# Kernel optimization log

Measured on AMD Instinct MI355X. Metric: run time of the kernel, lower is better.

Reference implementation:

```python
import jax, jax.numpy as jnp
import numpy as np

CNT_R = 500
DIM = 128
B, NEI = 8192, 64


def setup_inputs() -> dict:
    key = jax.random.key(0)
    ks = jax.random.split(key, 10)
    d2 = 2 * DIM
    return {
        "batch_nei_e_emb": jax.random.normal(ks[0], (B, NEI, DIM), dtype=jnp.float32),
        "batch_nei_rw": jax.random.uniform(ks[1], (B, NEI), dtype=jnp.float32),
        "w_r_table": jax.random.normal(ks[2], (2 * CNT_R + 1, DIM), dtype=jnp.float32),
        "zq_table": jax.random.normal(ks[3], (2 * CNT_R, DIM), dtype=jnp.float32),
        "attn_W_w": jax.random.normal(ks[4], (d2, d2), dtype=jnp.float32) / np.sqrt(d2),
        "attn_W_b": jnp.zeros((d2,), dtype=jnp.float32),
        "u_a_w": jax.random.normal(ks[5], (d2,), dtype=jnp.float32) / np.sqrt(d2),
        "u_a_b": jnp.zeros((), dtype=jnp.float32),
        "batch_nei_rid": jax.random.randint(ks[6], (B, NEI), 0, 2 * CNT_R + 1),
        "batch_q_rid": jax.random.randint(ks[7], (B,), 0, 2 * CNT_R),
    }


def reference(batch_nei_e_emb, batch_nei_rw, w_r_table, zq_table,
              attn_W_w, attn_W_b, u_a_w, u_a_b,
              batch_nei_rid, batch_q_rid):
    # gather relation hyperplane normals: (B, NEI, DIM)
    w_r = w_r_table[batch_nei_rid]
    n = w_r / jnp.linalg.norm(w_r, axis=-1, keepdims=True)
    # hyperplane projection: e - (e . n) n
    e = batch_nei_e_emb
    e_proj = e - jnp.sum(e * n, axis=-1, keepdims=True) * n
    # query relation embedding, tiled over neighbors: (B, NEI, DIM)
    z_q = zq_table[batch_q_rid]  # (B, DIM)
    z_q = jnp.broadcast_to(z_q[:, None, :], e_proj.shape)
    concat = jnp.concatenate([z_q, e_proj], axis=-1)  # (B, NEI, 2*DIM)
    h = jnp.tanh(jnp.einsum('bni,oi->bno', concat, attn_W_w) + attn_W_b)
    _alpha = jnp.einsum('bni,i->bn', h, u_a_w) + u_a_b  # (B, NEI)
    alpha = jax.nn.softmax(_alpha, axis=-1)
    attn = alpha + batch_nei_rw
    return attn
```

## Files before the change

kernel.cpp:

```cpp
#include <hip/hip_runtime.h>

#define NB    8192
#define NEI   64
#define DIM   128
#define D2    256
#define NR_W  1001
#define NR_Z  1000
#define EPB_LD 136

typedef __attribute__((ext_vector_type(8))) short bf16x8;
typedef __attribute__((ext_vector_type(4))) float f32x4;

__device__ __forceinline__ ushort f2bf(float x) {
    union { float f; unsigned u; } c; c.f = x;
    unsigned u = c.u;
    return (ushort)((u + 0x7fffu + ((u >> 16) & 1u)) >> 16);
}


__global__ void k_norm(const float* __restrict__ w_r_table, float* __restrict__ norm_t) {
    int r = blockIdx.x;
    int t = threadIdx.x;
    float v = w_r_table[r * DIM + t];
    float s = v * v;
    #pragma unroll
    for (int m = 1; m < 64; m <<= 1) s += __shfl_xor(s, m);
    __shared__ float sh[2];
    if ((t & 63) == 0) sh[t >> 6] = s;
    __syncthreads();
    float tot = sh[0] + sh[1];
    norm_t[r * DIM + t] = v / sqrtf(tot);
}

__global__ void k_tq(const float* __restrict__ zq_table, const float* __restrict__ W,
                     const float* __restrict__ bias, float* __restrict__ tq_t) {
    int r = blockIdx.x;
    int o = threadIdx.x;
    __shared__ float4 z4[32];
    if (o < 32) z4[o] = ((const float4*)(zq_table + r * DIM))[o];
    __syncthreads();
    const float4* wr = (const float4*)(W + o * D2);
    float acc = bias[o];
    #pragma unroll 8
    for (int i = 0; i < 32; ++i) {
        float4 wv = wr[i], zv = z4[i];
        acc += wv.x*zv.x + wv.y*zv.y + wv.z*zv.z + wv.w*zv.w;
    }
    tq_t[r * D2 + o] = acc;
}

__global__ void k_bfrag(const float* __restrict__ W, ushort* __restrict__ bfrag) {
    int nt = blockIdx.x;
    int kt = blockIdx.y;
    int l  = threadIdx.x;
    int o  = nt * 16 + (l & 15);
    int k  = kt * 32 + (l >> 4) * 8;
    const float4* src = (const float4*)(W + o * D2 + DIM + k);
    float4 a = src[0], c = src[1];
    uint4 w;
    w.x = f2bf(a.x) | ((unsigned)f2bf(a.y) << 16);
    w.y = f2bf(a.z) | ((unsigned)f2bf(a.w) << 16);
    w.z = f2bf(c.x) | ((unsigned)f2bf(c.y) << 16);
    w.w = f2bf(c.z) | ((unsigned)f2bf(c.w) << 16);
    *(uint4*)(bfrag + ((nt * 4 + kt) * 64 + l) * 8) = w;
}


__global__ __launch_bounds__(256) void k_main(
    const float* __restrict__ e_emb,
    const float* __restrict__ rw,
    const int*   __restrict__ nei_rid,
    const int*   __restrict__ q_rid,
    const float* __restrict__ norm_t,
    const float* __restrict__ tq_t,
    const ushort* __restrict__ bfrag,
    const float* __restrict__ u_a_w,
    float* __restrict__ out)
{
    __shared__ ushort ep16[NEI * EPB_LD];
    __shared__ float  alpw[4][NEI];

    const int b = blockIdx.x;
    const int t = threadIdx.x;
    const int wave = t >> 6, lane = t & 63;

    {
        const int row = t >> 2, q = t & 3;
        const float4* esrc = (const float4*)(e_emb + (size_t)b * NEI * DIM + row * DIM + q * 32);
        const int rid = nei_rid[b * NEI + row];
        const float4* nsrc = (const float4*)(norm_t + rid * DIM + q * 32);
        float4 ev[8], nv[8];
        #pragma unroll
        for (int i = 0; i < 8; ++i) { ev[i] = esrc[i]; nv[i] = nsrc[i]; }
        float part = 0.f;
        #pragma unroll
        for (int i = 0; i < 8; ++i)
            part += ev[i].x*nv[i].x + ev[i].y*nv[i].y + ev[i].z*nv[i].z + ev[i].w*nv[i].w;
        part += __shfl_xor(part, 1);
        part += __shfl_xor(part, 2);
        const float d = part;
        #pragma unroll
        for (int i = 0; i < 8; ++i) {
            ev[i].x -= d*nv[i].x; ev[i].y -= d*nv[i].y;
            ev[i].z -= d*nv[i].z; ev[i].w -= d*nv[i].w;
        }
        ushort* dst = &ep16[row * EPB_LD + q * 32];
        #pragma unroll
        for (int g = 0; g < 4; ++g) {
            float4 lo = ev[g*2], hi4 = ev[g*2+1];
            uint4 w;
            w.x = f2bf(lo.x)  | ((unsigned)f2bf(lo.y)  << 16);
            w.y = f2bf(lo.z)  | ((unsigned)f2bf(lo.w)  << 16);
            w.z = f2bf(hi4.x) | ((unsigned)f2bf(hi4.y) << 16);
            w.w = f2bf(hi4.z) | ((unsigned)f2bf(hi4.w) << 16);
            *(uint4*)(dst + g * 8) = w;
        }
    }

    const int ln = lane & 15, hi = lane >> 4;
    const int qr = q_rid[b];
    float tq4[4], ua4[4];
    #pragma unroll
    for (int nt = 0; nt < 4; ++nt) {
        int o = wave * 64 + nt * 16 + ln;
        tq4[nt] = tq_t[qr * D2 + o];
        ua4[nt] = u_a_w[o];
    }

    bf16x8 bfr_[4][4];
    #pragma unroll
    for (int nt = 0; nt < 4; ++nt)
        #pragma unroll
        for (int kt = 0; kt < 4; ++kt)
            bfr_[nt][kt] = *(const bf16x8*)(bfrag + (((wave*4 + nt)*4 + kt)*64 + lane)*8);

    __syncthreads();

    #pragma unroll
    for (int mt = 0; mt < 4; ++mt) {
        bf16x8 a_[4];
        #pragma unroll
        for (int kt = 0; kt < 4; ++kt)
            a_[kt] = *(const bf16x8*)&ep16[(mt*16 + ln) * EPB_LD + kt*32 + hi*8];
        f32x4 acc[4];
        #pragma unroll
        for (int nt = 0; nt < 4; ++nt) acc[nt] = (f32x4){0.f, 0.f, 0.f, 0.f};
        #pragma unroll
        for (int kt = 0; kt < 4; ++kt)
            #pragma unroll
            for (int nt = 0; nt < 4; ++nt)
                acc[nt] = __builtin_amdgcn_mfma_f32_16x16x32_bf16(a_[kt], bfr_[nt][kt], acc[nt], 0, 0, 0);
        float pr[4] = {0.f, 0.f, 0.f, 0.f};
        #pragma unroll
        for (int nt = 0; nt < 4; ++nt)
            #pragma unroll
            for (int j = 0; j < 4; ++j) {
                float v = acc[nt][j] + tq4[nt];
                float e2 = __expf(2.f * v);
                float h = 1.f - 2.f / (e2 + 1.f);
                pr[j] += ua4[nt] * h;
            }
        #pragma unroll
        for (int m = 1; m < 16; m <<= 1)
            #pragma unroll
            for (int j = 0; j < 4; ++j) pr[j] += __shfl_xor(pr[j], m);
        if (ln == 0) {
            #pragma unroll
            for (int j = 0; j < 4; ++j) alpw[wave][mt*16 + hi*4 + j] = pr[j];
        }
    }
    __syncthreads();

    if (t < NEI) {
        float a = alpw[0][t] + alpw[1][t] + alpw[2][t] + alpw[3][t];
        float mx = a;
        #pragma unroll
        for (int m = 1; m < 64; m <<= 1) mx = fmaxf(mx, __shfl_xor(mx, m));
        float p = __expf(a - mx);
        float s = p;
        #pragma unroll
        for (int m = 1; m < 64; m <<= 1) s += __shfl_xor(s, m);
        out[b * NEI + t] = p / s + rw[b * NEI + t];
    }
}


extern "C" void kernel_launch(void* const* d_in, const int* in_sizes, int n_in,
                              void* d_out, int out_size, void* d_ws, size_t ws_size,
                              hipStream_t stream) {
    const float* e_emb   = (const float*)d_in[0];
    const float* rw      = (const float*)d_in[1];
    const float* w_r_tab = (const float*)d_in[2];
    const float* zq_tab  = (const float*)d_in[3];
    const float* attn_W  = (const float*)d_in[4];
    const float* attn_b  = (const float*)d_in[5];
    const float* u_a_w   = (const float*)d_in[6];
    const int*   nei_rid = (const int*)d_in[8];
    const int*   q_rid   = (const int*)d_in[9];
    float* out = (float*)d_out;

    float* ws = (float*)d_ws;
    float* norm_t = ws;
    float* tq_t   = norm_t + NR_W * DIM;
    ushort* bfrag = (ushort*)(tq_t + NR_Z * D2);

    k_norm<<<NR_W, DIM, 0, stream>>>(w_r_tab, norm_t);
    k_tq<<<NR_Z, D2, 0, stream>>>(zq_tab, attn_W, attn_b, tq_t);
    k_bfrag<<<dim3(16, 4), 64, 0, stream>>>(attn_W, bfrag);
    k_main<<<NB, 256, 0, stream>>>(e_emb, rw, nei_rid, q_rid,
                                   norm_t, tq_t, bfrag, u_a_w, out);
}
```

Baseline: 147.9 us.

## Process four batches per block with register-prefetched embeddings

New measurement: 202.2 us. 1.37x slower.

```diff
diff --git a/kernel.cpp b/kernel.cpp
--- a/kernel.cpp
+++ b/kernel.cpp
@@ -7,6 +7,7 @@
 #define NR_W  1001
 #define NR_Z  1000
 #define EPB_LD 136
+#define BPB   4
 
 typedef __attribute__((ext_vector_type(8))) short bf16x8;
 typedef __attribute__((ext_vector_type(4))) float f32x4;
@@ -66,7 +67,7 @@
 }
 
 
-__global__ __launch_bounds__(256) void k_main(
+__global__ __launch_bounds__(256, 3) void k_main(
     const float* __restrict__ e_emb,
     const float* __restrict__ rw,
     const int*   __restrict__ nei_rid,
@@ -79,53 +80,23 @@
 {
     __shared__ ushort ep16[NEI * EPB_LD];
     __shared__ float  alpw[4][NEI];
-
-    const int b = blockIdx.x;
+    __shared__ int    rids_s[BPB * NEI];
+
+    const int b0 = blockIdx.x * BPB;
     const int t = threadIdx.x;
     const int wave = t >> 6, lane = t & 63;
-
-    {
-        const int row = t >> 2, q = t & 3;
-        const float4* esrc = (const float4*)(e_emb + (size_t)b * NEI * DIM + row * DIM + q * 32);
-        const int rid = nei_rid[b * NEI + row];
-        const float4* nsrc = (const float4*)(norm_t + rid * DIM + q * 32);
-        float4 ev[8], nv[8];
-        #pragma unroll
-        for (int i = 0; i < 8; ++i) { ev[i] = esrc[i]; nv[i] = nsrc[i]; }
-        float part = 0.f;
-        #pragma unroll
-        for (int i = 0; i < 8; ++i)
-            part += ev[i].x*nv[i].x + ev[i].y*nv[i].y + ev[i].z*nv[i].z + ev[i].w*nv[i].w;
-        part += __shfl_xor(part, 1);
-        part += __shfl_xor(part, 2);
-        const float d = part;
-        #pragma unroll
-        for (int i = 0; i < 8; ++i) {
-            ev[i].x -= d*nv[i].x; ev[i].y -= d*nv[i].y;
-            ev[i].z -= d*nv[i].z; ev[i].w -= d*nv[i].w;
-        }
-        ushort* dst = &ep16[row * EPB_LD + q * 32];
-        #pragma unroll
-        for (int g = 0; g < 4; ++g) {
-            float4 lo = ev[g*2], hi4 = ev[g*2+1];
-            uint4 w;
-            w.x = f2bf(lo.x)  | ((unsigned)f2bf(lo.y)  << 16);
-            w.y = f2bf(lo.z)  | ((unsigned)f2bf(lo.w)  << 16);
-            w.z = f2bf(hi4.x) | ((unsigned)f2bf(hi4.y) << 16);
-            w.w = f2bf(hi4.z) | ((unsigned)f2bf(hi4.w) << 16);
-            *(uint4*)(dst + g * 8) = w;
-        }
-    }
-
     const int ln = lane & 15, hi = lane >> 4;
-    const int qr = q_rid[b];
-    float tq4[4], ua4[4];
-    #pragma unroll
-    for (int nt = 0; nt < 4; ++nt) {
-        int o = wave * 64 + nt * 16 + ln;
-        tq4[nt] = tq_t[qr * D2 + o];
-        ua4[nt] = u_a_w[o];
-    }
+    const int row = t >> 2, q = t & 3;
+
+    int my_rid = nei_rid[b0 * NEI + t];
+
+    int qrs[BPB];
+    #pragma unroll
+    for (int i = 0; i < BPB; ++i) qrs[i] = q_rid[b0 + i];
+
+    float ua4[4];
+    #pragma unroll
+    for (int nt = 0; nt < 4; ++nt) ua4[nt] = u_a_w[wave * 64 + nt * 16 + ln];
 
     bf16x8 bfr_[4][4];
     #pragma unroll
@@ -134,53 +105,114 @@
         for (int kt = 0; kt < 4; ++kt)
             bfr_[nt][kt] = *(const bf16x8*)(bfrag + (((wave*4 + nt)*4 + kt)*64 + lane)*8);
 
+    rids_s[t] = my_rid;
+
+    float4 ev[2][8];
+    float  tq4p[2][4];
+    float  rwp[2];
+    {
+        const float4* esrc = (const float4*)(e_emb + ((size_t)b0 * NEI + row) * DIM + q * 32);
+        #pragma unroll
+        for (int k = 0; k < 8; ++k) ev[0][k] = esrc[k];
+        #pragma unroll
+        for (int nt = 0; nt < 4; ++nt) tq4p[0][nt] = tq_t[qrs[0] * D2 + wave*64 + nt*16 + ln];
+        rwp[0] = rw[(size_t)b0 * NEI + (t & 63)];
+    }
+
     __syncthreads();
 
     #pragma unroll
-    for (int mt = 0; mt < 4; ++mt) {
-        bf16x8 a_[4];
-        #pragma unroll
-        for (int kt = 0; kt < 4; ++kt)
-            a_[kt] = *(const bf16x8*)&ep16[(mt*16 + ln) * EPB_LD + kt*32 + hi*8];
-        f32x4 acc[4];
-        #pragma unroll
-        for (int nt = 0; nt < 4; ++nt) acc[nt] = (f32x4){0.f, 0.f, 0.f, 0.f};
-        #pragma unroll
-        for (int kt = 0; kt < 4; ++kt)
+    for (int i = 0; i < BPB; ++i) {
+        const int cur = i & 1, nxt = cur ^ 1;
+
+        {
+            const int rid = rids_s[i * NEI + row];
+            const float4* nsrc = (const float4*)(norm_t + rid * DIM + q * 32);
+            float4 nv[8];
+            #pragma unroll
+            for (int k = 0; k < 8; ++k) nv[k] = nsrc[k];
+            float part = 0.f;
+            #pragma unroll
+            for (int k = 0; k < 8; ++k) {
+                float4 e4 = ev[cur][k];
+                part += e4.x*nv[k].x + e4.y*nv[k].y + e4.z*nv[k].z + e4.w*nv[k].w;
+            }
+            part += __shfl_xor(part, 1);
+            part += __shfl_xor(part, 2);
+            const float d = part;
+            ushort* dst = &ep16[row * EPB_LD + q * 32];
+            #pragma unroll
+            for (int g = 0; g < 4; ++g) {
+                float4 lo = ev[cur][g*2], hi4 = ev[cur][g*2+1];
+                float4 nl = nv[g*2],     nh  = nv[g*2+1];
+                lo.x = fmaf(-d, nl.x, lo.x); lo.y = fmaf(-d, nl.y, lo.y);
+                lo.z = fmaf(-d, nl.z, lo.z); lo.w = fmaf(-d, nl.w, lo.w);
+                hi4.x = fmaf(-d, nh.x, hi4.x); hi4.y = fmaf(-d, nh.y, hi4.y);
+                hi4.z = fmaf(-d, nh.z, hi4.z); hi4.w = fmaf(-d, nh.w, hi4.w);
+                uint4 w;
+                w.x = f2bf(lo.x)  | ((unsigned)f2bf(lo.y)  << 16);
+                w.y = f2bf(lo.z)  | ((unsigned)f2bf(lo.w)  << 16);
+                w.z = f2bf(hi4.x) | ((unsigned)f2bf(hi4.y) << 16);
+                w.w = f2bf(hi4.z) | ((unsigned)f2bf(hi4.w) << 16);
+                *(uint4*)(dst + g * 8) = w;
+            }
+        }
+
+        if (i + 1 < BPB) {
+            const float4* esrc = (const float4*)(e_emb + ((size_t)(b0+i+1) * NEI + row) * DIM + q * 32);
+            #pragma unroll
+            for (int k = 0; k < 8; ++k) ev[nxt][k] = esrc[k];
+            #pragma unroll
+            for (int nt = 0; nt < 4; ++nt) tq4p[nxt][nt] = tq_t[qrs[i+1] * D2 + wave*64 + nt*16 + ln];
+            rwp[nxt] = rw[(size_t)(b0+i+1) * NEI + (t & 63)];
+        }
+
+        __syncthreads();
+
+        #pragma unroll
+        for (int mt = 0; mt < 4; ++mt) {
+            bf16x8 a_[4];
+            #pragma unroll
+            for (int kt = 0; kt < 4; ++kt)
+                a_[kt] = *(const bf16x8*)&ep16[(mt*16 + ln) * EPB_LD + kt*32 + hi*8];
+            f32x4 acc[4];
+            #pragma unroll
+            for (int nt = 0; nt < 4; ++nt) acc[nt] = (f32x4){0.f, 0.f, 0.f, 0.f};
+            #pragma unroll
+            for (int kt = 0; kt < 4; ++kt)
+                #pragma unroll
+                for (int nt = 0; nt < 4; ++nt)
+                    acc[nt] = __builtin_amdgcn_mfma_f32_16x16x32_bf16(a_[kt], bfr_[nt][kt], acc[nt], 0, 0, 0);
+            float pr[4] = {0.f, 0.f, 0.f, 0.f};
             #pragma unroll
             for (int nt = 0; nt < 4; ++nt)
-                acc[nt] = __builtin_amdgcn_mfma_f32_16x16x32_bf16(a_[kt], bfr_[nt][kt], acc[nt], 0, 0, 0);
-        float pr[4] = {0.f, 0.f, 0.f, 0.f};
-        #pragma unroll
-        for (int nt = 0; nt < 4; ++nt)
-            #pragma unroll
-            for (int j = 0; j < 4; ++j) {
-                float v = acc[nt][j] + tq4[nt];
-                float e2 = __expf(2.f * v);
-                float h = 1.f - 2.f / (e2 + 1.f);
-                pr[j] += ua4[nt] * h;
+                #pragma unroll
+                for (int j = 0; j < 4; ++j) {
+                    float v = acc[nt][j] + tq4p[cur][nt];
+                    float e2 = __expf(2.f * v);
+                    float r  = __builtin_amdgcn_rcpf(e2 + 1.f);
+                    float h  = fmaf(-2.f, r, 1.f);
+                    pr[j] += ua4[nt] * h;
+                }
+            #pragma unroll
+            for (int m = 1; m < 16; m <<= 1)
+                #pragma unroll
+                for (int j = 0; j < 4; ++j) pr[j] += __shfl_xor(pr[j], m);
+            if (ln == 0) {
+                #pragma unroll
+                for (int j = 0; j < 4; ++j) alpw[wave][mt*16 + hi*4 + j] = pr[j];
             }
-        #pragma unroll
-        for (int m = 1; m < 16; m <<= 1)
-            #pragma unroll
-            for (int j = 0; j < 4; ++j) pr[j] += __shfl_xor(pr[j], m);
-        if (ln == 0) {
-            #pragma unroll
-            for (int j = 0; j < 4; ++j) alpw[wave][mt*16 + hi*4 + j] = pr[j];
-        }
-    }
-    __syncthreads();
-
-    if (t < NEI) {
-        float a = alpw[0][t] + alpw[1][t] + alpw[2][t] + alpw[3][t];
-        float mx = a;
-        #pragma unroll
-        for (int m = 1; m < 64; m <<= 1) mx = fmaxf(mx, __shfl_xor(mx, m));
-        float p = __expf(a - mx);
-        float s = p;
-        #pragma unroll
-        for (int m = 1; m < 64; m <<= 1) s += __shfl_xor(s, m);
-        out[b * NEI + t] = p / s + rw[b * NEI + t];
+        }
+        __syncthreads();
+
+        if (t < NEI) {
+            float a = alpw[0][t] + alpw[1][t] + alpw[2][t] + alpw[3][t];
+            float p = __expf(a);
+            float s = p;
+            #pragma unroll
+            for (int m = 1; m < 64; m <<= 1) s += __shfl_xor(s, m);
+            out[(size_t)(b0 + i) * NEI + t] = fmaf(p, __builtin_amdgcn_rcpf(s), rwp[cur]);
+        }
     }
 }
 
@@ -207,6 +239,6 @@
     k_norm<<<NR_W, DIM, 0, stream>>>(w_r_tab, norm_t);
     k_tq<<<NR_Z, D2, 0, stream>>>(zq_tab, attn_W, attn_b, tq_t);
     k_bfrag<<<dim3(16, 4), 64, 0, stream>>>(attn_W, bfrag);
-    k_main<<<NB, 256, 0, stream>>>(e_emb, rw, nei_rid, q_rid,
-                                   norm_t, tq_t, bfrag, u_a_w, out);
-}
+    k_main<<<NB / BPB, 256, 0, stream>>>(e_emb, rw, nei_rid, q_rid,
+                                         norm_t, tq_t, bfrag, u_a_w, out);
+}
```
